# Kernel optimization log

Measured on AMD Instinct MI355X. Metric: run time of the kernel, lower is better.

The kernel has to match this reference:

```python
import jax, jax.numpy as jnp
import numpy as np

B, NNODES, NODE, EDGEF, HID, NFACT, DEG = 256, 64, 64, 32, 256, 8, 32
N_TOTAL = B * NNODES            # 16384 nodes
E_TOTAL = B * NNODES * DEG      # 524288 edges
NEDGES_HEAD = 128               # len(self.edges)


def _w(key, shape, fan_in):
    return jax.random.normal(key, shape, dtype=jnp.float32) * (1.0 / np.sqrt(fan_in))


def setup_inputs() -> dict:
    key = jax.random.key(0)
    ks = jax.random.split(key, 16)
    # message-passing edge_index: per graph, node i -> (i+k) % NNODES, k=1..DEG
    src = np.repeat(np.arange(NNODES), DEG)
    dst = (src + np.tile(np.arange(1, DEG + 1), NNODES)) % NNODES
    offs = (np.arange(B) * NNODES)[:, None]
    ei = np.stack([(src[None, :] + offs).reshape(-1),
                   (dst[None, :] + offs).reshape(-1)], axis=0)
    edge_index = jnp.asarray(ei, dtype=jnp.int32)  # [2, E_TOTAL]
    # actor head edge list (within-graph indices): ring distance 1 and 2
    e1 = np.stack([np.arange(NNODES), (np.arange(NNODES) + 1) % NNODES], 1)
    e2 = np.stack([np.arange(NNODES), (np.arange(NNODES) + 2) % NNODES], 1)
    edges = jnp.asarray(np.concatenate([e1, e2], 0), dtype=jnp.int32)  # [128,2]

    D = NODE + HID  # 320
    inp = {
        "x": jax.random.normal(ks[0], (N_TOTAL, NODE), dtype=jnp.float32),
        "edge_index": edge_index,
        "edge_attr": jax.random.normal(ks[1], (E_TOTAL, EDGEF), dtype=jnp.float32),
        "edges": edges,
        "high": jax.random.uniform(ks[2], (NEDGES_HEAD + NFACT,), minval=0.5, maxval=2.0),
        "W1": _w(ks[3], (2 * NODE + EDGEF, HID), 2 * NODE + EDGEF),
        "b1": jnp.zeros((HID,), jnp.float32),
        "W2": _w(ks[4], (HID, HID), HID),
        "b2": jnp.zeros((HID,), jnp.float32),
        "Wmu": _w(ks[5], (2 * D, 1), 2 * D),
        "bmu": jnp.zeros((1,), jnp.float32),
        "Wsig": _w(ks[6], (2 * D, 1), 2 * D),
        "bsig": jnp.zeros((1,), jnp.float32),
        "Wmu2": _w(ks[7], (D, 1), D),
        "bmu2": jnp.zeros((1,), jnp.float32),
        "Wsig2": _w(ks[8], (D, 1), D),
        "bsig2": jnp.zeros((1,), jnp.float32),
    }
    return inp


def reference(x, edge_index, edge_attr, edges, high,
              W1, b1, W2, b2, Wmu, bmu, Wsig, bsig, Wmu2, bmu2, Wsig2, bsig2):
    # EdgeConv (flow='target_to_source', aggr='add'): x_i=x[ei0], x_j=x[ei1], aggregate at ei0
    xi = x[edge_index[0]]                                   # [E, NODE]
    xj = x[edge_index[1]]                                   # [E, NODE]
    msg_in = jnp.concatenate([xi, xj, edge_attr], axis=1)   # [E, 2*NODE+EDGEF]
    msg = jax.nn.relu(msg_in @ W1 + b1) @ W2 + b2           # [E, HID]
    agg = jax.ops.segment_sum(msg, edge_index[0], num_segments=x.shape[0])  # [N, HID]

    x_pp = jnp.concatenate([x, agg], axis=1).reshape(-1, NNODES, NODE + HID)  # [B, nn, D]

    ef_src = x_pp[:, edges[:, 0], :]                        # [B, 128, D]
    ef_dst = x_pp[:, edges[:, 1], :]                        # [B, 128, D]
    ef = jnp.concatenate([ef_src, ef_dst], axis=2)          # [B, 128, 2D]

    alpha = jax.nn.softplus((ef @ Wmu + bmu).squeeze(-1) + 1e-20)    # [B, 128]
    beta = jax.nn.softplus((ef @ Wsig + bsig).squeeze(-1) + 1e-20)   # [B, 128]

    fact = x_pp[:, -NFACT:, :]                              # [B, 8, D]
    alpha2 = jax.nn.softplus((fact @ Wmu2 + bmu2).squeeze(-1) + 1e-20)   # [B, 8]
    beta2 = jax.nn.softplus((fact @ Wsig2 + bsig2).squeeze(-1) + 1e-20)  # [B, 8]

    # deterministic=True path
    alpha = alpha + 1e-20
    beta = beta + 1e-20
    dis_action = alpha / (alpha + beta) * high[:-NFACT]     # [B, 128]
    alpha2 = alpha2 + 1e-20
    beta2 = beta2 + 1e-20
    order_act = alpha2 / (alpha2 + beta2) * high[-NFACT:]   # [B, 8]
    act = jnp.concatenate([dis_action, order_act], axis=-1) # [B, 136]
    return act
```

## Files before the change

kernel.cpp:

```cpp
#include <hip/hip_runtime.h>
#include <math.h>

#define BATCH_  256
#define NTOT    16384
#define ETOT    524288

typedef __attribute__((ext_vector_type(8))) short short8v;
typedef __attribute__((ext_vector_type(4))) float f32x4;

#define MFMA16(a,b,c) __builtin_amdgcn_mfma_f32_16x16x32_bf16((a),(b),(c),0,0,0)

__device__ __forceinline__ unsigned short f2bf(float f) {
    unsigned int x = __float_as_uint(f);
    return (unsigned short)((x + 0x7fffu + ((x >> 16) & 1u)) >> 16);
}
__device__ __forceinline__ float bf2f(unsigned short h) {
    return __uint_as_float(((unsigned int)h) << 16);
}
__device__ __forceinline__ float softplus_f(float v) {
    return v > 20.f ? v : log1pf(expf(v));
}
__device__ __forceinline__ float dot4(f32x4 a, f32x4 b) {
    float z = a[0] * b[0];
    z = fmaf(a[1], b[1], z);
    z = fmaf(a[2], b[2], z);
    z = fmaf(a[3], b[3], z);
    return z;
}
__device__ __forceinline__ void packfrag(f32x4 a, f32x4 q, short8v& hi, short8v& lo) {
    float v[8] = {a[0], a[1], a[2], a[3], q[0], q[1], q[2], q[3]};
#pragma unroll
    for (int j = 0; j < 8; j++) {
        const unsigned short h = f2bf(v[j]);
        hi[j] = (short)h;
        lo[j] = (short)f2bf(v[j] - bf2f(h));
    }
}
__device__ __forceinline__ short8v cvthi8(f32x4 a, f32x4 q) {
    union { short8v s; unsigned int u[4]; } r;
    asm("v_cvt_pk_bf16_f32 %0, %1, %2" : "=v"(r.u[0]) : "v"(a[0]), "v"(a[1]));
    asm("v_cvt_pk_bf16_f32 %0, %1, %2" : "=v"(r.u[1]) : "v"(a[2]), "v"(a[3]));
    asm("v_cvt_pk_bf16_f32 %0, %1, %2" : "=v"(r.u[2]) : "v"(q[0]), "v"(q[1]));
    asm("v_cvt_pk_bf16_f32 %0, %1, %2" : "=v"(r.u[3]) : "v"(q[2]), "v"(q[3]));
    return r.s;
}

__global__ __launch_bounds__(256) void k_prep(const float* __restrict__ W1,
                                              const float* __restrict__ W2,
                                              unsigned short* __restrict__ frags) {
    const int u = blockIdx.x;
    const float* S = (u < 80) ? W1 : W2;
    const int ul = (u < 80) ? u : (u - 80);
    const int rowbase = (ul >> 4) * 32;
    const int cht = ul & 15;
    for (int idx = threadIdx.x; idx < 512; idx += 256) {
        const int l = idx >> 3, j = idx & 7;
        const int row = rowbase + ((l >> 4) << 3) + j;
        const int col = cht * 16 + (l & 15);
        const float v = S[row * 256 + col];
        const unsigned short h = f2bf(v);
        frags[u * 1024 + idx]       = h;
        frags[u * 1024 + 512 + idx] = f2bf(v - bf2f(h));
    }
}

__global__ __launch_bounds__(512) __attribute__((amdgpu_waves_per_eu(2)))
void k_ab3(
    const float* __restrict__ x, const float* __restrict__ ea,
    const int* __restrict__ dst, const float* __restrict__ b1,
    const unsigned short* __restrict__ frags, float* __restrict__ sumh1)
{
    __shared__ __align__(16) unsigned char smem[67584];
    float*          s_xwb  = (float*)smem;
    unsigned short* s_ea   = (unsigned short*)(smem + 32768);
    unsigned char*  s_dstl = (unsigned char*)(smem + 65536);

    const int b = blockIdx.x & 255, half = blockIdx.x >> 8;
    const int tid = threadIdx.x;
    const int l = tid & 63, w = tid >> 6, g = l >> 4, l15 = l & 15;
    const int ng = w & 3, cqq = w >> 2;
    const int node = ng * 16 + l15;
    const int swzn = (l15 & 7) << 2;

    for (int idx = tid; idx < 2048; idx += 512)
        s_dstl[idx] = (unsigned char)(dst[b * 2048 + idx] & 63);

    const int sns = tid >> 3;
    const int so4 = (tid & 7) >> 1;
    const int sg0 = (tid & 1) * 2;
    const int snl = sns & 15, ssng = sns >> 4;
    const float* seab = ea + (size_t)b * 65536 + (size_t)sns * 1024
                           + so4 * 32 + (tid & 1) * 16;

    f32x4 L0 = *(const f32x4*)(seab);
    f32x4 L1 = *(const f32x4*)(seab + 4);
    f32x4 L2 = *(const f32x4*)(seab + 8);
    f32x4 L3 = *(const f32x4*)(seab + 12);

    short8v Xh[2], Xl[2];
#pragma unroll
    for (int kt = 0; kt < 2; kt++) {
        const float* p = x + (size_t)(b * 64 + node) * 64 + kt * 32 + g * 8;
        packfrag(*(const f32x4*)p, *(const f32x4*)(p + 4), Xh[kt], Xl[kt]);
    }

    f32x4 xab1[4];
#pragma unroll
    for (int i = 0; i < 4; i++) {
        const int cht = half * 8 + cqq * 4 + i;
        f32x4 d = *(const f32x4*)&b1[cht * 16 + g * 4];
#pragma unroll
        for (int kt = 0; kt < 2; kt++) {
            const int base = (kt * 16 + cht) * 1024 + l * 8;
            const short8v Ahh = *(const short8v*)&frags[base];
            const short8v All = *(const short8v*)&frags[base + 512];
            d = MFMA16(All, Xh[kt], d);
            d = MFMA16(Ahh, Xl[kt], d);
            d = MFMA16(Ahh, Xh[kt], d);
        }
        xab1[i] = d;
    }

#pragma unroll
    for (int i = 0; i < 4; i++) {
        const int cht = half * 8 + cqq * 4 + i;
        f32x4 d = {0.f, 0.f, 0.f, 0.f};
#pragma unroll
        for (int kt = 0; kt < 2; kt++) {
            const int base = ((kt + 2) * 16 + cht) * 1024 + l * 8;
            const short8v Ahh = *(const short8v*)&frags[base];
            const short8v All = *(const short8v*)&frags[base + 512];
            d = MFMA16(All, Xh[kt], d);
            d = MFMA16(Ahh, Xl[kt], d);
            d = MFMA16(Ahh, Xh[kt], d);
        }
        *(f32x4*)&s_xwb[node * 128 + (((cqq * 4 + i) * 16 + g * 4) ^ swzn)] = d;
    }

    short8v Ah[4], Al[4];
#pragma unroll
    for (int i = 0; i < 4; i++) {
        const int base = (64 + half * 8 + cqq * 4 + i) * 1024 + l * 8;
        Ah[i] = *(const short8v*)&frags[base];
        Al[i] = *(const short8v*)&frags[base + 512];
    }

    {
        unsigned short* p = s_ea + ((0 * 4 + so4) * 4 + ssng) * 512;
        *(short8v*)&p[(sg0 * 16 + snl) * 8]       = cvthi8(L0, L1);
        *(short8v*)&p[((sg0 + 1) * 16 + snl) * 8] = cvthi8(L2, L3);
    }
    L0 = *(const f32x4*)(seab + 128);
    L1 = *(const f32x4*)(seab + 132);
    L2 = *(const f32x4*)(seab + 136);
    L3 = *(const f32x4*)(seab + 140);
    __syncthreads();

    f32x4 acc[4];
#pragma unroll
    for (int i = 0; i < 4; i++) acc[i] = (f32x4){0.f, 0.f, 0.f, 0.f};

    for (int c = 0; c < 8; ++c) {
        if (c < 7) {
            const int nb = (c + 1) & 1;
            unsigned short* p = s_ea + ((nb * 4 + so4) * 4 + ssng) * 512;
            *(short8v*)&p[(sg0 * 16 + snl) * 8]       = cvthi8(L0, L1);
            *(short8v*)&p[((sg0 + 1) * 16 + snl) * 8] = cvthi8(L2, L3);
            if (c < 6) {
                const float* q = seab + (size_t)(c + 2) * 128;
                L0 = *(const f32x4*)(q);
                L1 = *(const f32x4*)(q + 4);
                L2 = *(const f32x4*)(q + 8);
                L3 = *(const f32x4*)(q + 12);
            }
        }

        const int cb = c & 1;
        const unsigned int dw = ((const unsigned int*)s_dstl)[node * 8 + c];

#pragma unroll
        for (int ol = 0; ol < 4; ol++) {
            const short8v Bh =
                *(const short8v*)&s_ea[((cb * 4 + ol) * 4 + ng) * 512 + l * 8];
            const int d = (dw >> (ol * 8)) & 63;
            const int swz = (d & 7) << 2;

#pragma unroll
            for (int i = 0; i < 4; i++) {
                const int cbl = (cqq * 4 + i) * 16 + g * 4;
                const f32x4 wb = *(const f32x4*)&s_xwb[d * 128 + (cbl ^ swz)];
                f32x4 di = MFMA16(Al[i], Bh, xab1[i]);
                di = MFMA16(Ah[i], Bh, di);
#pragma unroll
                for (int r = 0; r < 4; r++)
                    acc[i][r] += fmaxf(di[r] + wb[r], 0.f);
            }
        }
        __syncthreads();
    }

    const size_t grow = (size_t)b * 64 + node;
#pragma unroll
    for (int i = 0; i < 4; i++) {
        const int cg = (half * 8 + cqq * 4 + i) * 16 + g * 4;
        *(f32x4*)&sumh1[grow * 256 + cg] = acc[i];
    }
}

__global__ __launch_bounds__(1024) __attribute__((amdgpu_waves_per_eu(2)))
void k_cd2(
    const float* __restrict__ x, const float* __restrict__ sumh1,
    const int* __restrict__ edges, const float* __restrict__ high,
    const unsigned short* __restrict__ frags, const float* __restrict__ b2,
    const float* __restrict__ Wmu,  const float* __restrict__ bmu,
    const float* __restrict__ Wsig, const float* __restrict__ bsig,
    const float* __restrict__ Wmu2, const float* __restrict__ bmu2,
    const float* __restrict__ Wsig2,const float* __restrict__ bsig2,
    float* __restrict__ out)
{
    __shared__ __align__(16) unsigned char smem[131072];
    float* s_sumh1 = (float*)smem;
    float* s_agg   = (float*)(smem + 65536);
    float* s_su    = (float*)smem;
    float* s_su2   = (float*)(smem + 1024);
    float* s_w     = (float*)(smem + 2048);

    const int b = blockIdx.x, tid = threadIdx.x;
    const int l = tid & 63, w = tid >> 6, g = l >> 4, l15 = l & 15;
    const int swzn = (l15 & 7) << 2;

    for (int idx = tid; idx < 4096; idx += 1024) {
        const int row = idx >> 6, c4 = (idx & 63) * 4;
        const f32x4 v = *(const f32x4*)&sumh1[(size_t)b * 16384 + (size_t)idx * 4];
        *(f32x4*)&s_sumh1[row * 256 + (c4 ^ ((row & 7) << 2))] = v;
    }
    __syncthreads();

    const int rt = w & 3, cj = w >> 2;
    f32x4 acc2[4];
#pragma unroll
    for (int j = 0; j < 4; j++) acc2[j] = (f32x4){0.f, 0.f, 0.f, 0.f};

    for (int ks = 0; ks < 8; ks++) {
        const int row = rt * 16 + l15;
        const int cbk = ks * 32 + g * 8;
        const f32x4 a0 = *(const f32x4*)&s_sumh1[row * 256 + (cbk ^ swzn)];
        const f32x4 a1 = *(const f32x4*)&s_sumh1[row * 256 + ((cbk + 4) ^ swzn)];
        short8v Ahh, All;
        packfrag(a0, a1, Ahh, All);
#pragma unroll
        for (int j = 0; j < 4; j++) {
            const int base = (80 + ks * 16 + cj * 4 + j) * 1024 + l * 8;
            const short8v Bh = *(const short8v*)&frags[base];
            const short8v Bl = *(const short8v*)&frags[base + 512];
            acc2[j] = MFMA16(Ahh, Bh, acc2[j]);
            acc2[j] = MFMA16(Ahh, Bl, acc2[j]);
            acc2[j] = MFMA16(All, Bh, acc2[j]);
        }
    }

#pragma unroll
    for (int j = 0; j < 4; j++) {
        const int col = (cj * 4 + j) * 16 + l15;
        const float bb = 32.f * b2[col];
#pragma unroll
        for (int r = 0; r < 4; r++) {
            const int row = rt * 16 + g * 4 + r;
            s_agg[row * 256 + (col ^ ((row & 7) << 2))] = acc2[j][r] + bb;
        }
    }
    __syncthreads();

    for (int i = tid; i < 1920; i += 1024)
        s_w[i] = (i < 640) ? Wmu[i]
               : (i < 1280) ? Wsig[i - 640]
               : (i < 1600) ? Wmu2[i - 1280] : Wsig2[i - 1600];
    __syncthreads();

    if (tid < 256) {
        const int n = tid >> 2, s = tid & 3;
        const float* Wp = s_w + (s & 1) * 640 + ((s >> 1) ? 320 : 0);
        const float* xr = x + (size_t)(b * 64 + n) * 64;
        const int sw = (n & 7) << 2;
        float z = 0.f;
#pragma unroll
        for (int kq = 0; kq < 16; kq++)
            z += dot4(*(const f32x4*)&xr[kq * 4], *(const f32x4*)&Wp[kq * 4]);
#pragma unroll 8
        for (int kq = 0; kq < 64; kq++)
            z += dot4(*(const f32x4*)&s_agg[n * 256 + ((kq * 4) ^ sw)],
                      *(const f32x4*)&Wp[64 + kq * 4]);
        s_su[n * 4 + s] = z;
    } else if (tid < 272) {
        const int j = (tid - 256) >> 1, s = tid & 1;
        const int n = 56 + j;
        const float* Wp = s_w + 1280 + (s ? 320 : 0);
        const float* xr = x + (size_t)(b * 64 + n) * 64;
        const int sw = (n & 7) << 2;
        float z = 0.f;
#pragma unroll
        for (int kq = 0; kq < 16; kq++)
            z += dot4(*(const f32x4*)&xr[kq * 4], *(const f32x4*)&Wp[kq * 4]);
#pragma unroll 8
        for (int kq = 0; kq < 64; kq++)
            z += dot4(*(const f32x4*)&s_agg[n * 256 + ((kq * 4) ^ sw)],
                      *(const f32x4*)&Wp[64 + kq * 4]);
        s_su2[j * 2 + s] = z;
    }
    __syncthreads();

    if (tid < 128) {
        const int e0 = edges[tid * 2], e1 = edges[tid * 2 + 1];
        const float a  = softplus_f(s_su[e0 * 4 + 0] + s_su[e1 * 4 + 2] + bmu[0])  + 1e-20f;
        const float be = softplus_f(s_su[e0 * 4 + 1] + s_su[e1 * 4 + 3] + bsig[0]) + 1e-20f;
        out[(size_t)b * 136 + tid] = a / (a + be) * high[tid];
    } else if (tid < 136) {
        const int j = tid - 128;
        const float a  = softplus_f(s_su2[j * 2 + 0] + bmu2[0])  + 1e-20f;
        const float be = softplus_f(s_su2[j * 2 + 1] + bsig2[0]) + 1e-20f;
        out[(size_t)b * 136 + tid] = a / (a + be) * high[128 + j];
    }
}

extern "C" void kernel_launch(void* const* d_in, const int* in_sizes, int n_in,
                              void* d_out, int out_size, void* d_ws, size_t ws_size,
                              hipStream_t stream) {
    const float* x     = (const float*)d_in[0];
    const int*   eidx  = (const int*)  d_in[1];
    const float* ea    = (const float*)d_in[2];
    const int*   edges = (const int*)  d_in[3];
    const float* high  = (const float*)d_in[4];
    const float* W1    = (const float*)d_in[5];
    const float* b1    = (const float*)d_in[6];
    const float* W2    = (const float*)d_in[7];
    const float* b2    = (const float*)d_in[8];
    const float* Wmu   = (const float*)d_in[9];
    const float* bmu   = (const float*)d_in[10];
    const float* Wsig  = (const float*)d_in[11];
    const float* bsig  = (const float*)d_in[12];
    const float* Wmu2  = (const float*)d_in[13];
    const float* bmu2  = (const float*)d_in[14];
    const float* Wsig2 = (const float*)d_in[15];
    const float* bsig2 = (const float*)d_in[16];
    float* out = (float*)d_out;

    float* sumh1 = (float*)d_ws;
    const size_t frag_off = (ws_size - (size_t)208 * 2048) & ~(size_t)1023;
    unsigned short* frags = (unsigned short*)((char*)d_ws + frag_off);
    const int* dst = eidx + ETOT;

    hipLaunchKernelGGL(k_prep, dim3(208),    dim3(256),  0, stream, W1, W2, frags);
    hipLaunchKernelGGL(k_ab3,  dim3(512),    dim3(512),  0, stream,
                       x, ea, dst, b1, frags, sumh1);
    hipLaunchKernelGGL(k_cd2,  dim3(BATCH_), dim3(1024), 0, stream,
                       x, sumh1, edges, high, frags, b2,
                       Wmu, bmu, Wsig, bsig, Wmu2, bmu2, Wsig2, bsig2, out);
}
```

Measured before the change: 73.24 us.

## Split edge-message kernel over two edge halves with partial-sum reduction in consumer

The edge-message kernel now launches twice as many blocks, each handling half of every node's outgoing edges (16 of 32). Each block writes its partial sums into one of two sumh1 buffers, and the second kernel adds the two partials when it loads them. The aim is more parallelism and occupancy, since shared memory per block shrinks and the grid is larger. The cost is redundant per-block setup (X·W products, weight fragment loads), twice the sumh1 write and read traffic, and a larger workspace requirement.

```diff
diff --git a/kernel.cpp b/kernel.cpp
--- a/kernel.cpp
+++ b/kernel.cpp
@@ -65,17 +65,18 @@
 }
 
 __global__ __launch_bounds__(512) __attribute__((amdgpu_waves_per_eu(2)))
-void k_ab3(
+void k_ab4(
     const float* __restrict__ x, const float* __restrict__ ea,
     const int* __restrict__ dst, const float* __restrict__ b1,
     const unsigned short* __restrict__ frags, float* __restrict__ sumh1)
 {
-    __shared__ __align__(16) unsigned char smem[67584];
+    __shared__ __align__(16) unsigned char smem[51200];
     float*          s_xwb  = (float*)smem;
     unsigned short* s_ea   = (unsigned short*)(smem + 32768);
-    unsigned char*  s_dstl = (unsigned char*)(smem + 65536);
-
-    const int b = blockIdx.x & 255, half = blockIdx.x >> 8;
+    unsigned char*  s_dstl = (unsigned char*)(smem + 49152);
+
+    const int bx = blockIdx.x;
+    const int b = bx & 255, half = (bx >> 8) & 1, oh = bx >> 9;
     const int tid = threadIdx.x;
     const int l = tid & 63, w = tid >> 6, g = l >> 4, l15 = l & 15;
     const int ng = w & 3, cqq = w >> 2;
@@ -86,16 +87,14 @@
         s_dstl[idx] = (unsigned char)(dst[b * 2048 + idx] & 63);
 
     const int sns = tid >> 3;
-    const int so4 = (tid & 7) >> 1;
-    const int sg0 = (tid & 1) * 2;
+    const int so  = (tid & 7) >> 2;
+    const int ko  = tid & 3;
     const int snl = sns & 15, ssng = sns >> 4;
     const float* seab = ea + (size_t)b * 65536 + (size_t)sns * 1024
-                           + so4 * 32 + (tid & 1) * 16;
+                           + (oh * 16 + so) * 32 + ko * 8;
 
     f32x4 L0 = *(const f32x4*)(seab);
     f32x4 L1 = *(const f32x4*)(seab + 4);
-    f32x4 L2 = *(const f32x4*)(seab + 8);
-    f32x4 L3 = *(const f32x4*)(seab + 12);
 
     short8v Xh[2], Xl[2];
 #pragma unroll
@@ -145,15 +144,10 @@
         Al[i] = *(const short8v*)&frags[base + 512];
     }
 
-    {
-        unsigned short* p = s_ea + ((0 * 4 + so4) * 4 + ssng) * 512;
-        *(short8v*)&p[(sg0 * 16 + snl) * 8]       = cvthi8(L0, L1);
-        *(short8v*)&p[((sg0 + 1) * 16 + snl) * 8] = cvthi8(L2, L3);
-    }
-    L0 = *(const f32x4*)(seab + 128);
-    L1 = *(const f32x4*)(seab + 132);
-    L2 = *(const f32x4*)(seab + 136);
-    L3 = *(const f32x4*)(seab + 140);
+    *(short8v*)&s_ea[((0 * 2 + so) * 4 + ssng) * 512 + (ko * 16 + snl) * 8]
+        = cvthi8(L0, L1);
+    L0 = *(const f32x4*)(seab + 64);
+    L1 = *(const f32x4*)(seab + 68);
     __syncthreads();
 
     f32x4 acc[4];
@@ -163,26 +157,24 @@
     for (int c = 0; c < 8; ++c) {
         if (c < 7) {
             const int nb = (c + 1) & 1;
-            unsigned short* p = s_ea + ((nb * 4 + so4) * 4 + ssng) * 512;
-            *(short8v*)&p[(sg0 * 16 + snl) * 8]       = cvthi8(L0, L1);
-            *(short8v*)&p[((sg0 + 1) * 16 + snl) * 8] = cvthi8(L2, L3);
+            *(short8v*)&s_ea[((nb * 2 + so) * 4 + ssng) * 512 + (ko * 16 + snl) * 8]
+                = cvthi8(L0, L1);
             if (c < 6) {
-                const float* q = seab + (size_t)(c + 2) * 128;
+                const float* q = seab + (size_t)(c + 2) * 64;
                 L0 = *(const f32x4*)(q);
                 L1 = *(const f32x4*)(q + 4);
-                L2 = *(const f32x4*)(q + 8);
-                L3 = *(const f32x4*)(q + 12);
             }
         }
 
         const int cb = c & 1;
-        const unsigned int dw = ((const unsigned int*)s_dstl)[node * 8 + c];
-
-#pragma unroll
-        for (int ol = 0; ol < 4; ol++) {
+        const unsigned short dwc =
+            *(const unsigned short*)&s_dstl[node * 32 + oh * 16 + c * 2];
+
+#pragma unroll
+        for (int ol = 0; ol < 2; ol++) {
             const short8v Bh =
-                *(const short8v*)&s_ea[((cb * 4 + ol) * 4 + ng) * 512 + l * 8];
-            const int d = (dw >> (ol * 8)) & 63;
+                *(const short8v*)&s_ea[((cb * 2 + ol) * 4 + ng) * 512 + l * 8];
+            const int d = (dwc >> (ol * 8)) & 63;
             const int swz = (d & 7) << 2;
 
 #pragma unroll
@@ -199,11 +191,11 @@
         __syncthreads();
     }
 
-    const size_t grow = (size_t)b * 64 + node;
+    float* outp = sumh1 + (size_t)oh * NTOT * 256 + ((size_t)b * 64 + node) * 256;
 #pragma unroll
     for (int i = 0; i < 4; i++) {
         const int cg = (half * 8 + cqq * 4 + i) * 16 + g * 4;
-        *(f32x4*)&sumh1[grow * 256 + cg] = acc[i];
+        *(f32x4*)&outp[cg] = acc[i];
     }
 }
 
@@ -231,8 +223,10 @@
 
     for (int idx = tid; idx < 4096; idx += 1024) {
         const int row = idx >> 6, c4 = (idx & 63) * 4;
-        const f32x4 v = *(const f32x4*)&sumh1[(size_t)b * 16384 + (size_t)idx * 4];
-        *(f32x4*)&s_sumh1[row * 256 + (c4 ^ ((row & 7) << 2))] = v;
+        const f32x4 v0 = *(const f32x4*)&sumh1[(size_t)b * 16384 + (size_t)idx * 4];
+        const f32x4 v1 = *(const f32x4*)&sumh1[(size_t)NTOT * 256 +
+                                               (size_t)b * 16384 + (size_t)idx * 4];
+        *(f32x4*)&s_sumh1[row * 256 + (c4 ^ ((row & 7) << 2))] = v0 + v1;
     }
     __syncthreads();
 
@@ -350,7 +344,7 @@
     const int* dst = eidx + ETOT;
 
     hipLaunchKernelGGL(k_prep, dim3(208),    dim3(256),  0, stream, W1, W2, frags);
-    hipLaunchKernelGGL(k_ab3,  dim3(512),    dim3(512),  0, stream,
+    hipLaunchKernelGGL(k_ab4,  dim3(1024),   dim3(512),  0, stream,
                        x, ea, dst, b1, frags, sumh1);
     hipLaunchKernelGGL(k_cd2,  dim3(BATCH_), dim3(1024), 0, stream,
                        x, sumh1, edges, high, frags, b2,
```

New measurement: 90.70 us. 1.24x slower.
